# Optimization experiments

Measured on AMD Instinct MI355X. Metric: run time of the kernel, lower is better.

The kernel has to match this reference:

```python
import jax, jax.numpy as jnp
import numpy as np

N, E = 50000, 800000
F_IN, H, P, C = 128, 64, 16, 40
L = 3  # gcn_layers


def setup_inputs() -> dict:
    key = jax.random.key(0)
    ks = jax.random.split(key, 10)
    s = 0.05
    return {
        "x_h": jax.random.normal(ks[0], (N, F_IN), jnp.float32),
        "pos_feat": jax.random.normal(ks[1], (N, P), jnp.float32),
        "edge_index": jax.random.randint(ks[2], (2, E), 0, N, dtype=jnp.int32),
        "W_pos": jax.random.normal(ks[3], (P, H), jnp.float32) * s,
        "b_pos": jnp.zeros((H,), jnp.float32),
        "W_init": jax.random.normal(ks[4], (F_IN, H), jnp.float32) * s,
        "b_init": jnp.zeros((H,), jnp.float32),
        "W_l": jax.random.normal(ks[5], (L, H, H), jnp.float32) * s,  # neighbor weight
        "W_r": jax.random.normal(ks[6], (L, H, H), jnp.float32) * s,  # root weight
        "b_conv": jnp.zeros((L, H), jnp.float32),
        "W_last": jax.random.normal(ks[7], (H, C), jnp.float32) * s,
        "b_last": jnp.zeros((C,), jnp.float32),
    }


def _sage_conv(x, src, dst, Wl, Wr, b):
    # PyG SAGEConv(aggr='mean'): out_i = Wl @ mean_{j in N(i)} x_j + Wr @ x_i + b
    msgs = x[src]  # [E, H] gather of source-node features
    agg = jax.ops.segment_sum(msgs, dst, num_segments=N)
    cnt = jax.ops.segment_sum(jnp.ones((E,), x.dtype), dst, num_segments=N)
    agg = agg / jnp.clip(cnt, 1.0, None)[:, None]  # mean; deg-0 nodes -> 0
    return agg @ Wl + x @ Wr + b


def reference(x_h, pos_feat, edge_index, W_pos, b_pos, W_init, b_init,
              W_l, W_r, b_conv, W_last, b_last):
    src, dst = edge_index[0], edge_index[1]
    # pos_embedding -> (hyperbolic encode simplified to identity in Euclidean manifold) -> tanh
    hyp_pos = jnp.tanh(pos_feat @ W_pos + b_pos)  # [N, H]
    h = x_h @ W_init + b_init  # [N, H]
    for i in range(L):
        h = _sage_conv(h, src, dst, W_l[i], W_r[i], b_conv[i])
        if i != L - 1:
            h = h + hyp_pos       # run_base == 'False' branch
            h = jax.nn.relu(h)    # dropout is no-op in eval mode
    emb = h @ W_last + b_last     # [N, C]
    return emb, jax.nn.log_softmax(emb, axis=1)
```

## Files before the change

### kernel.cpp

```cpp
#include <hip/hip_runtime.h>
#include <hip/hip_bf16.h>

#define NN 50000
#define NE 800000
#define FIN 128
#define HD 64
#define NC 40
#define XG   782
#define NB   391
#define NBK  782
#define BW   64
#define BSTR 2048
#define GGRID 1563

typedef __hip_bfloat16 bf16;
typedef __attribute__((ext_vector_type(8))) short bf16x8;
typedef __attribute__((ext_vector_type(4))) float f32x4;

__device__ __forceinline__ void acc8(float* a, uint4 v){
  a[0] += __uint_as_float(v.x << 16); a[1] += __uint_as_float(v.x & 0xffff0000u);
  a[2] += __uint_as_float(v.y << 16); a[3] += __uint_as_float(v.y & 0xffff0000u);
  a[4] += __uint_as_float(v.z << 16); a[5] += __uint_as_float(v.z & 0xffff0000u);
  a[6] += __uint_as_float(v.w << 16); a[7] += __uint_as_float(v.w & 0xffff0000u);
}

__device__ __forceinline__ unsigned pack2(float lo, float hi){
  union { bf16 b; unsigned short u; } a, b;
  a.b = __float2bfloat16(lo);
  b.b = __float2bfloat16(hi);
  return (unsigned)a.u | ((unsigned)b.u << 16);
}

__device__ __forceinline__ short f2bf_bits(float f){
  union { bf16 b; short s; } u;
  u.b = __float2bfloat16(f);
  return u.s;
}

__device__ __forceinline__ void init_body(
    int wid, const float* __restrict__ x, const float* __restrict__ pos,
    const float* __restrict__ Wi, const float* __restrict__ bi,
    const float* __restrict__ Wp, const float* __restrict__ bp,
    bf16* __restrict__ h0b, bf16* __restrict__ hypb, int lane){
  const int quad = lane >> 4;
  const int col  = lane & 15;
  const int nw   = XG * 4;

  bf16x8 wif[4][4];
  #pragma unroll
  for (int ct = 0; ct < 4; ++ct)
    #pragma unroll
    for (int kf = 0; kf < 4; ++kf)
      #pragma unroll
      for (int j = 0; j < 8; ++j)
        wif[ct][kf][j] = f2bf_bits(Wi[(kf*32 + quad*8 + j)*HD + ct*16 + col]);
  bf16x8 wpf[4];
  #pragma unroll
  for (int ct = 0; ct < 4; ++ct)
    #pragma unroll
    for (int j = 0; j < 8; ++j){
      const int k = quad*8 + j;
      wpf[ct][j] = (k < 16) ? f2bf_bits(Wp[k*HD + ct*16 + col]) : (short)0;
    }
  float bih[4], bph[4];
  #pragma unroll
  for (int c = 0; c < 4; ++c){ bih[c] = bi[c*16 + col]; bph[c] = bp[c*16 + col]; }

  for (int t = wid; t < NN/16; t += nw){
    const int n0 = t * 16;
    bf16x8 af[4];
    #pragma unroll
    for (int kf = 0; kf < 4; ++kf){
      const float* xr = x + (size_t)(n0 + col)*FIN + kf*32 + quad*8;
      const float4 f0 = *(const float4*)xr;
      const float4 f1 = *(const float4*)(xr + 4);
      af[kf][0] = f2bf_bits(f0.x); af[kf][1] = f2bf_bits(f0.y);
      af[kf][2] = f2bf_bits(f0.z); af[kf][3] = f2bf_bits(f0.w);
      af[kf][4] = f2bf_bits(f1.x); af[kf][5] = f2bf_bits(f1.y);
      af[kf][6] = f2bf_bits(f1.z); af[kf][7] = f2bf_bits(f1.w);
    }
    bf16x8 ap;
    #pragma unroll
    for (int j = 0; j < 8; ++j) ap[j] = 0;
    if (quad < 2){
      const float* pr = pos + (size_t)(n0 + col)*16 + quad*8;
      const float4 p0 = *(const float4*)pr;
      const float4 p1 = *(const float4*)(pr + 4);
      ap[0] = f2bf_bits(p0.x); ap[1] = f2bf_bits(p0.y);
      ap[2] = f2bf_bits(p0.z); ap[3] = f2bf_bits(p0.w);
      ap[4] = f2bf_bits(p1.x); ap[5] = f2bf_bits(p1.y);
      ap[6] = f2bf_bits(p1.z); ap[7] = f2bf_bits(p1.w);
    }
    f32x4 ah[4], app[4];
    #pragma unroll
    for (int c = 0; c < 4; ++c){
      ah[c]  = (f32x4){bih[c], bih[c], bih[c], bih[c]};
      app[c] = (f32x4){bph[c], bph[c], bph[c], bph[c]};
    }
    #pragma unroll
    for (int ct = 0; ct < 4; ++ct){
      #pragma unroll
      for (int kf = 0; kf < 4; ++kf)
        ah[ct] = __builtin_amdgcn_mfma_f32_16x16x32_bf16(af[kf], wif[ct][kf], ah[ct], 0, 0, 0);
      app[ct] = __builtin_amdgcn_mfma_f32_16x16x32_bf16(ap, wpf[ct], app[ct], 0, 0, 0);
    }
    #pragma unroll
    for (int reg = 0; reg < 4; ++reg){
      const int n = n0 + quad*4 + reg;
      #pragma unroll
      for (int c = 0; c < 4; ++c){
        h0b[(size_t)n*HD + c*16 + col]  = __float2bfloat16(ah[c][reg]);
        hypb[(size_t)n*HD + c*16 + col] = __float2bfloat16(tanhf(app[c][reg]));
      }
    }
  }
}

__global__ __launch_bounds__(256) void k_hist(
    const int* __restrict__ ei, int* __restrict__ histT,
    const float* __restrict__ x, const float* __restrict__ pos,
    const float* __restrict__ Wi, const float* __restrict__ bi,
    const float* __restrict__ Wp, const float* __restrict__ bp,
    bf16* __restrict__ h0b, bf16* __restrict__ hypb){
  __shared__ int lh[NBK];
  if (blockIdx.x < NB){
    for (int i = threadIdx.x; i < NBK; i += 256) lh[i] = 0;
    __syncthreads();
    int e = blockIdx.x * 2048 + threadIdx.x;
    #pragma unroll
    for (int j = 0; j < 8; ++j, e += 256)
      if (e < NE) atomicAdd(&lh[ei[NE + e] >> 6], 1);
    __syncthreads();
    for (int i = threadIdx.x; i < NBK; i += 256)
      histT[blockIdx.x*NBK + i] = lh[i];
    return;
  }
  init_body((blockIdx.x - NB) * 4 + (threadIdx.x >> 6),
            x, pos, Wi, bi, Wp, bp, h0b, hypb, threadIdx.x & 63);
}

__global__ __launch_bounds__(512) void k_scanA(
    const int* __restrict__ histT, int* __restrict__ ofsT,
    int* __restrict__ totals){
  __shared__ int sc[512];
  const int b = blockIdx.x;
  const int t = threadIdx.x;
  const int v = (t < NB) ? histT[t*NBK + b] : 0;
  sc[t] = v; __syncthreads();
  for (int off = 1; off < 512; off <<= 1){
    const int xv = (t >= off) ? sc[t - off] : 0;
    __syncthreads();
    sc[t] += xv;
    __syncthreads();
  }
  if (t < NB) ofsT[t*NBK + b] = sc[t] - v;
  if (t == 511) totals[b] = sc[511];
}

__global__ __launch_bounds__(256) void k_scatter(
    const int* __restrict__ ei, const int* __restrict__ ofsT,
    int* __restrict__ packed){
  __shared__ int cur[NBK];
  for (int i = threadIdx.x; i < NBK; i += 256)
    cur[i] = (i << 11) + ofsT[blockIdx.x*NBK + i];
  __syncthreads();
  int e = blockIdx.x * 2048 + threadIdx.x;
  #pragma unroll
  for (int j = 0; j < 8; ++j, e += 256){
    if (e < NE){
      const int d = ei[NE + e];
      const int s = ei[e];
      const int b = d >> 6;
      const int p = atomicAdd(&cur[b], 1);
      if (p < ((b + 1) << 11))
        packed[p] = s | ((d & 63) << 16);
    }
  }
}

__global__ __launch_bounds__(256) void k_ell(
    const int* __restrict__ packed, const int* __restrict__ totals,
    unsigned short* __restrict__ esrc, int* __restrict__ degp){
  __shared__ int cnt[BW];
  __shared__ unsigned short ell[BW * 64];
  if (threadIdx.x < BW) cnt[threadIdx.x] = 0;
  __syncthreads();
  const int b  = blockIdx.x;
  const int lo = b << 11;
  const int hi = lo + totals[b];
  for (int e = lo + threadIdx.x; e < hi; e += 256){
    const int pk = packed[e];
    const int dl = (pk >> 16) & 63;
    const int p  = atomicAdd(&cnt[dl], 1);
    if (p < 64) ell[dl*64 + p] = (unsigned short)(pk & 0xffff);
  }
  __syncthreads();
  const int n0 = b * BW;
  for (int i = threadIdx.x; i < BW * 8; i += 256){
    const int node = i >> 3;
    if (n0 + node < NN)
      ((uint4*)(esrc + (size_t)(n0 + node)*64))[i & 7] = ((const uint4*)ell)[i];
  }
  for (int i = threadIdx.x; i < BW; i += 256)
    if (n0 + i < NN) degp[n0 + i] = min(cnt[i], 64);
}


__device__ __forceinline__ bf16x8 lds_frag(const unsigned int* hs, int r, int slot){
  union { uint4 u; bf16x8 v; } t;
  t.u = *(const uint4*)(hs + r*32 + ((slot ^ (r & 7)) << 2));
  return t.v;
}

__device__ __forceinline__ void gather_own_stage(
    const bf16* __restrict__ h, const int* __restrict__ degp,
    const unsigned short* __restrict__ esrc, unsigned int* hs){
  const int lane = threadIdx.x & 63;
  const int w    = threadIdx.x >> 6;
  const int grp  = lane >> 3;
  const int fq   = lane & 7;
  const int nl   = (w << 3) + grp;
  const int n    = (blockIdx.x << 5) + nl;
  const int ns   = (n < NN) ? n : 0;
  const int deg  = (n < NN) ? min(degp[n], 64) : 0;

  const uint4 hv = ((const uint4*)(h + (size_t)ns*HD))[fq];
  *(uint4*)(hs + 1024 + nl*32 + ((fq ^ (nl & 7)) << 2)) = hv;

  const uint4* er = (const uint4*)(esrc + ((size_t)ns << 6));
  float a[8] = {0,0,0,0,0,0,0,0};
  for (int eb = 0; eb < 64; eb += 8){
    if (!__any(eb < deg)) break;
    union { uint4 u; unsigned short s[8]; } ev;
    ev.u = er[eb >> 3];
    const int m = deg - eb;
    #pragma unroll
    for (int j = 0; j < 8; ++j){
      if (j < m){
        const uint4 v = ((const uint4*)(h + (size_t)ev.s[j]*HD))[fq];
        acc8(a, v);
      }
    }
  }
  const float inv = deg > 0 ? 1.f / (float)deg : 0.f;
  uint4 pv;
  pv.x = pack2(a[0]*inv, a[1]*inv);
  pv.y = pack2(a[2]*inv, a[3]*inv);
  pv.z = pack2(a[4]*inv, a[5]*inv);
  pv.w = pack2(a[6]*inv, a[7]*inv);
  *(uint4*)(hs + nl*32 + ((fq ^ (nl & 7)) << 2)) = pv;
}

__global__ __launch_bounds__(256) void k_g(
    const bf16* __restrict__ h, const int* __restrict__ degp,
    const unsigned short* __restrict__ esrc,
    const float* __restrict__ Wl, const float* __restrict__ Wr,
    const float* __restrict__ bc, const bf16* __restrict__ hypb,
    bf16* __restrict__ ho){
  __shared__ unsigned int hs[2048];
  const int lane = threadIdx.x & 63;
  const int w    = threadIdx.x >> 6;
  const int quad = lane >> 4;
  const int col  = lane & 15;
  const int tile = w & 1;
  const int ch   = w >> 1;

  bf16x8 fw[2][4];
  float zb[2];
  #pragma unroll
  for (int c = 0; c < 2; ++c){
    const int nc = (ch*2 + c)*16 + col;
    zb[c] = bc[nc];
    #pragma unroll
    for (int kf = 0; kf < 4; ++kf)
      #pragma unroll
      for (int j = 0; j < 8; ++j){
        const int k = kf*32 + quad*8 + j;
        fw[c][kf][j] = f2bf_bits((k < 64) ? Wl[k*HD + nc] : Wr[(k - 64)*HD + nc]);
      }
  }

  gather_own_stage(h, degp, esrc, hs);
  __syncthreads();

  const int r = tile*16 + col;
  const bf16x8 a0 = lds_frag(hs, r, quad);
  const bf16x8 a1 = lds_frag(hs, r, quad + 4);
  const bf16x8 a2 = lds_frag(hs + 1024, r, quad);
  const bf16x8 a3 = lds_frag(hs + 1024, r, quad + 4);
  __syncthreads();

  const int n0b = blockIdx.x << 5;
  unsigned short* st = (unsigned short*)hs;
  f32x4 acc[2];
  #pragma unroll
  for (int c = 0; c < 2; ++c){
    acc[c] = (f32x4){zb[c], zb[c], zb[c], zb[c]};
    acc[c] = __builtin_amdgcn_mfma_f32_16x16x32_bf16(a0, fw[c][0], acc[c], 0, 0, 0);
    acc[c] = __builtin_amdgcn_mfma_f32_16x16x32_bf16(a1, fw[c][1], acc[c], 0, 0, 0);
    acc[c] = __builtin_amdgcn_mfma_f32_16x16x32_bf16(a2, fw[c][2], acc[c], 0, 0, 0);
    acc[c] = __builtin_amdgcn_mfma_f32_16x16x32_bf16(a3, fw[c][3], acc[c], 0, 0, 0);
  }
  #pragma unroll
  for (int reg = 0; reg < 4; ++reg){
    const int rr = tile*16 + quad*4 + reg;
    const int nn = n0b + rr;
    #pragma unroll
    for (int c = 0; c < 2; ++c){
      const int oc = (ch*2 + c)*16 + col;
      float v = acc[c][reg];
      if (nn < NN) v += __bfloat162float(hypb[(size_t)nn*HD + oc]);
      v = fmaxf(v, 0.f);
      st[rr*64 + (((oc >> 3) ^ (rr & 7)) << 3) + (oc & 7)] = (unsigned short)f2bf_bits(v);
    }
  }
  __syncthreads();
  const int grp = lane >> 3;
  const int fq  = lane & 7;
  const int nl  = (w << 3) + grp;
  const int n   = n0b + nl;
  if (n < NN)
    ((uint4*)(ho + (size_t)n*HD))[fq] = *(const uint4*)(hs + nl*32 + ((fq ^ (nl & 7)) << 2));
}

__global__ __launch_bounds__(256) void k_gf(
    const bf16* __restrict__ h, const int* __restrict__ degp,
    const unsigned short* __restrict__ esrc,
    const float* __restrict__ Wl, const float* __restrict__ Wr,
    const float* __restrict__ bc,
    const float* __restrict__ Wlast, const float* __restrict__ blast,
    float* __restrict__ out){
  __shared__ unsigned int hs[2048];
  const int lane = threadIdx.x & 63;
  const int w    = threadIdx.x >> 6;
  const int quad = lane >> 4;
  const int col  = lane & 15;
  const int tile = w & 1;
  const int ch   = w >> 1;

  bf16x8 fw[2][4];
  float zb[2];
  #pragma unroll
  for (int c = 0; c < 2; ++c){
    const int nc = (ch*2 + c)*16 + col;
    zb[c] = bc[nc];
    #pragma unroll
    for (int kf = 0; kf < 4; ++kf)
      #pragma unroll
      for (int j = 0; j < 8; ++j){
        const int k = kf*32 + quad*8 + j;
        fw[c][kf][j] = f2bf_bits((k < 64) ? Wl[k*HD + nc] : Wr[(k - 64)*HD + nc]);
      }
  }

  gather_own_stage(h, degp, esrc, hs);
  __syncthreads();

  const int r = tile*16 + col;
  const bf16x8 a0 = lds_frag(hs, r, quad);
  const bf16x8 a1 = lds_frag(hs, r, quad + 4);
  const bf16x8 a2 = lds_frag(hs + 1024, r, quad);
  const bf16x8 a3 = lds_frag(hs + 1024, r, quad + 4);
  __syncthreads();

  const int n0b = blockIdx.x << 5;
  unsigned short* st = (unsigned short*)hs;
  f32x4 acc[2];
  #pragma unroll
  for (int c = 0; c < 2; ++c){
    acc[c] = (f32x4){zb[c], zb[c], zb[c], zb[c]};
    acc[c] = __builtin_amdgcn_mfma_f32_16x16x32_bf16(a0, fw[c][0], acc[c], 0, 0, 0);
    acc[c] = __builtin_amdgcn_mfma_f32_16x16x32_bf16(a1, fw[c][1], acc[c], 0, 0, 0);
    acc[c] = __builtin_amdgcn_mfma_f32_16x16x32_bf16(a2, fw[c][2], acc[c], 0, 0, 0);
    acc[c] = __builtin_amdgcn_mfma_f32_16x16x32_bf16(a3, fw[c][3], acc[c], 0, 0, 0);
  }
  #pragma unroll
  for (int reg = 0; reg < 4; ++reg){
    const int rr = tile*16 + quad*4 + reg;
    #pragma unroll
    for (int c = 0; c < 2; ++c){
      const int oc = (ch*2 + c)*16 + col;
      st[rr*64 + (((oc >> 3) ^ (rr & 7)) << 3) + (oc & 7)] =
          (unsigned short)f2bf_bits(acc[c][reg]);
    }
  }
  __syncthreads();
  if (w >= 2) return;

  bf16x8 wf[3][2];
  float bb[3];
  #pragma unroll
  for (int ct = 0; ct < 3; ++ct){
    const int nc = ct*16 + col;
    const bool valid = nc < NC;
    bb[ct] = valid ? blast[nc] : -1e30f;
    #pragma unroll
    for (int kf = 0; kf < 2; ++kf)
      #pragma unroll
      for (int j = 0; j < 8; ++j)
        wf[ct][kf][j] = valid ? f2bf_bits(Wlast[(kf*32 + quad*8 + j)*NC + nc]) : (short)0;
  }
  const int r2 = w*16 + col;
  const bf16x8 b0 = lds_frag(hs, r2, quad);
  const bf16x8 b1 = lds_frag(hs, r2, quad + 4);
  f32x4 ac[3];
  #pragma unroll
  for (int ct = 0; ct < 3; ++ct){
    ac[ct] = (f32x4){bb[ct], bb[ct], bb[ct], bb[ct]};
    ac[ct] = __builtin_amdgcn_mfma_f32_16x16x32_bf16(b0, wf[ct][0], ac[ct], 0, 0, 0);
    ac[ct] = __builtin_amdgcn_mfma_f32_16x16x32_bf16(b1, wf[ct][1], ac[ct], 0, 0, 0);
  }
  #pragma unroll
  for (int reg = 0; reg < 4; ++reg){
    const float e0 = ac[0][reg], e1 = ac[1][reg], e2 = ac[2][reg];
    float vmax = fmaxf(fmaxf(e0, e1), e2);
    vmax = fmaxf(vmax, __shfl_xor(vmax, 1, 64));
    vmax = fmaxf(vmax, __shfl_xor(vmax, 2, 64));
    vmax = fmaxf(vmax, __shfl_xor(vmax, 4, 64));
    vmax = fmaxf(vmax, __shfl_xor(vmax, 8, 64));
    float s = __expf(e0 - vmax) + __expf(e1 - vmax) + __expf(e2 - vmax);
    s += __shfl_xor(s, 1, 64);
    s += __shfl_xor(s, 2, 64);
    s += __shfl_xor(s, 4, 64);
    s += __shfl_xor(s, 8, 64);
    const float off = vmax + __logf(s);
    const int n = n0b + w*16 + quad*4 + reg;
    if (n < NN){
      #pragma unroll
      for (int ct = 0; ct < 3; ++ct){
        const int nc = ct*16 + col;
        if (nc < NC){
          const float e = ac[ct][reg];
          out[(size_t)n*NC + nc]                 = e;
          out[(size_t)NN*NC + (size_t)n*NC + nc] = e - off;
        }
      }
    }
  }
}

extern "C" void kernel_launch(void* const* d_in, const int* in_sizes, int n_in,
                              void* d_out, int out_size, void* d_ws, size_t ws_size,
                              hipStream_t stream){
  (void)in_sizes; (void)n_in; (void)out_size; (void)ws_size;
  const float* x_h    = (const float*)d_in[0];
  const float* pos    = (const float*)d_in[1];
  const int*   ei     = (const int*)  d_in[2];
  const float* W_pos  = (const float*)d_in[3];
  const float* b_pos  = (const float*)d_in[4];
  const float* W_init = (const float*)d_in[5];
  const float* b_init = (const float*)d_in[6];
  const float* W_l    = (const float*)d_in[7];
  const float* W_r    = (const float*)d_in[8];
  const float* b_conv = (const float*)d_in[9];
  const float* W_last = (const float*)d_in[10];
  const float* b_last = (const float*)d_in[11];
  float* out = (float*)d_out;

  char* p = (char*)d_ws;
  auto alloc = [&](size_t bytes)->char*{
    char* r = p; p += (bytes + 255) & ~(size_t)255; return r;
  };
  bf16* buf0 = (bf16*)alloc((size_t)NN*HD*2);
  bf16* buf1 = (bf16*)alloc((size_t)NN*HD*2);
  bf16* hypb = (bf16*)alloc((size_t)NN*HD*2);
  unsigned short* esrc = (unsigned short*)alloc((size_t)NN*64*2);
  int* degp   = (int*)alloc((size_t)NN*4);
  int* histT  = (int*)alloc((size_t)NB*NBK*4);
  int* ofsT   = (int*)alloc((size_t)NB*NBK*4);
  int* totals = (int*)alloc((size_t)NBK*4);
  int* packed = (int*)alloc((size_t)NBK*BSTR*4);

  k_hist   <<<NB + XG, 256, 0, stream>>>(ei, histT, x_h, pos,
                                         W_init, b_init, W_pos, b_pos, buf0, hypb);
  k_scanA  <<<NBK, 512, 0, stream>>>(histT, ofsT, totals);
  k_scatter<<<NB, 256, 0, stream>>>(ei, ofsT, packed);
  k_ell    <<<NBK, 256, 0, stream>>>(packed, totals, esrc, degp);

  k_g  <<<GGRID, 256, 0, stream>>>(buf0, degp, esrc,
                                   W_l + 0*HD*HD, W_r + 0*HD*HD, b_conv + 0*HD,
                                   hypb, buf1);
  k_g  <<<GGRID, 256, 0, stream>>>(buf1, degp, esrc,
                                   W_l + 1*HD*HD, W_r + 1*HD*HD, b_conv + 1*HD,
                                   hypb, buf0);
  k_gf <<<GGRID, 256, 0, stream>>>(buf0, degp, esrc,
                                   W_l + 2*HD*HD, W_r + 2*HD*HD, b_conv + 2*HD,
                                   W_last, b_last, out);
}
```

Before: 240.7 us.

## Fuse three SAGE layer kernels into one persistent kernel with grid barriers

Replaces the three per-layer kernel launches with a single persistent kernel of 512 blocks that loops over the node tiles and uses a software grid-wide barrier between layers. It removes two launches and the drain/fill gaps between them, and weights are loaded once per block rather than per tile. In exchange, parallelism drops from 1563 blocks to 512 with grid-stride loops, and correctness depends on all 512 blocks being co-resident, since the spin barrier deadlocks otherwise.

```diff
diff --git a/kernel.cpp b/kernel.cpp
--- a/kernel.cpp
+++ b/kernel.cpp
@@ -12,6 +12,7 @@
 #define BW   64
 #define BSTR 2048
 #define GGRID 1563
+#define LGRID 512
 
 typedef __hip_bfloat16 bf16;
 typedef __attribute__((ext_vector_type(8))) short bf16x8;
@@ -35,6 +36,24 @@
   union { bf16 b; short s; } u;
   u.b = __float2bfloat16(f);
   return u.s;
+}
+
+__device__ __forceinline__ void gridbar(int* bar, int* gen, const int nblk){
+  __syncthreads();
+  if (threadIdx.x == 0){
+    __threadfence();
+    const int g = __hip_atomic_load(gen, __ATOMIC_RELAXED, __HIP_MEMORY_SCOPE_AGENT);
+    const int v = __hip_atomic_fetch_add(bar, 1, __ATOMIC_ACQ_REL, __HIP_MEMORY_SCOPE_AGENT);
+    if (v == nblk - 1){
+      __hip_atomic_store(bar, 0, __ATOMIC_RELAXED, __HIP_MEMORY_SCOPE_AGENT);
+      __hip_atomic_fetch_add(gen, 1, __ATOMIC_RELEASE, __HIP_MEMORY_SCOPE_AGENT);
+    } else {
+      while (__hip_atomic_load(gen, __ATOMIC_RELAXED, __HIP_MEMORY_SCOPE_AGENT) == g)
+        __builtin_amdgcn_s_sleep(2);
+    }
+    __threadfence();
+  }
+  __syncthreads();
 }
 
 __device__ __forceinline__ void init_body(
@@ -205,7 +224,6 @@
     if (n0 + i < NN) degp[n0 + i] = min(cnt[i], 64);
 }
 
-
 __device__ __forceinline__ bf16x8 lds_frag(const unsigned int* hs, int r, int slot){
   union { uint4 u; bf16x8 v; } t;
   t.u = *(const uint4*)(hs + r*32 + ((slot ^ (r & 7)) << 2));
@@ -214,13 +232,13 @@
 
 __device__ __forceinline__ void gather_own_stage(
     const bf16* __restrict__ h, const int* __restrict__ degp,
-    const unsigned short* __restrict__ esrc, unsigned int* hs){
+    const unsigned short* __restrict__ esrc, unsigned int* hs, int tb){
   const int lane = threadIdx.x & 63;
   const int w    = threadIdx.x >> 6;
   const int grp  = lane >> 3;
   const int fq   = lane & 7;
   const int nl   = (w << 3) + grp;
-  const int n    = (blockIdx.x << 5) + nl;
+  const int n    = (tb << 5) + nl;
   const int ns   = (n < NN) ? n : 0;
   const int deg  = (n < NN) ? min(degp[n], 64) : 0;
 
@@ -251,13 +269,12 @@
   *(uint4*)(hs + nl*32 + ((fq ^ (nl & 7)) << 2)) = pv;
 }
 
-__global__ __launch_bounds__(256) void k_g(
-    const bf16* __restrict__ h, const int* __restrict__ degp,
+__device__ __forceinline__ void layer_body(
+    unsigned int* hs, const bf16* __restrict__ h, const int* __restrict__ degp,
     const unsigned short* __restrict__ esrc,
     const float* __restrict__ Wl, const float* __restrict__ Wr,
     const float* __restrict__ bc, const bf16* __restrict__ hypb,
     bf16* __restrict__ ho){
-  __shared__ unsigned int hs[2048];
   const int lane = threadIdx.x & 63;
   const int w    = threadIdx.x >> 6;
   const int quad = lane >> 4;
@@ -280,161 +297,173 @@
       }
   }
 
-  gather_own_stage(h, degp, esrc, hs);
-  __syncthreads();
-
-  const int r = tile*16 + col;
-  const bf16x8 a0 = lds_frag(hs, r, quad);
-  const bf16x8 a1 = lds_frag(hs, r, quad + 4);
-  const bf16x8 a2 = lds_frag(hs + 1024, r, quad);
-  const bf16x8 a3 = lds_frag(hs + 1024, r, quad + 4);
-  __syncthreads();
-
-  const int n0b = blockIdx.x << 5;
-  unsigned short* st = (unsigned short*)hs;
-  f32x4 acc[2];
-  #pragma unroll
-  for (int c = 0; c < 2; ++c){
-    acc[c] = (f32x4){zb[c], zb[c], zb[c], zb[c]};
-    acc[c] = __builtin_amdgcn_mfma_f32_16x16x32_bf16(a0, fw[c][0], acc[c], 0, 0, 0);
-    acc[c] = __builtin_amdgcn_mfma_f32_16x16x32_bf16(a1, fw[c][1], acc[c], 0, 0, 0);
-    acc[c] = __builtin_amdgcn_mfma_f32_16x16x32_bf16(a2, fw[c][2], acc[c], 0, 0, 0);
-    acc[c] = __builtin_amdgcn_mfma_f32_16x16x32_bf16(a3, fw[c][3], acc[c], 0, 0, 0);
-  }
-  #pragma unroll
-  for (int reg = 0; reg < 4; ++reg){
-    const int rr = tile*16 + quad*4 + reg;
-    const int nn = n0b + rr;
+  for (int tb = blockIdx.x; tb < GGRID; tb += LGRID){
+    gather_own_stage(h, degp, esrc, hs, tb);
+    __syncthreads();
+    const int r = tile*16 + col;
+    const bf16x8 a0 = lds_frag(hs, r, quad);
+    const bf16x8 a1 = lds_frag(hs, r, quad + 4);
+    const bf16x8 a2 = lds_frag(hs + 1024, r, quad);
+    const bf16x8 a3 = lds_frag(hs + 1024, r, quad + 4);
+    __syncthreads();
+
+    const int n0b = tb << 5;
+    unsigned short* st = (unsigned short*)hs;
+    f32x4 acc[2];
     #pragma unroll
     for (int c = 0; c < 2; ++c){
-      const int oc = (ch*2 + c)*16 + col;
-      float v = acc[c][reg];
-      if (nn < NN) v += __bfloat162float(hypb[(size_t)nn*HD + oc]);
-      v = fmaxf(v, 0.f);
-      st[rr*64 + (((oc >> 3) ^ (rr & 7)) << 3) + (oc & 7)] = (unsigned short)f2bf_bits(v);
-    }
-  }
-  __syncthreads();
-  const int grp = lane >> 3;
-  const int fq  = lane & 7;
-  const int nl  = (w << 3) + grp;
-  const int n   = n0b + nl;
-  if (n < NN)
-    ((uint4*)(ho + (size_t)n*HD))[fq] = *(const uint4*)(hs + nl*32 + ((fq ^ (nl & 7)) << 2));
-}
-
-__global__ __launch_bounds__(256) void k_gf(
-    const bf16* __restrict__ h, const int* __restrict__ degp,
+      acc[c] = (f32x4){zb[c], zb[c], zb[c], zb[c]};
+      acc[c] = __builtin_amdgcn_mfma_f32_16x16x32_bf16(a0, fw[c][0], acc[c], 0, 0, 0);
+      acc[c] = __builtin_amdgcn_mfma_f32_16x16x32_bf16(a1, fw[c][1], acc[c], 0, 0, 0);
+      acc[c] = __builtin_amdgcn_mfma_f32_16x16x32_bf16(a2, fw[c][2], acc[c], 0, 0, 0);
+      acc[c] = __builtin_amdgcn_mfma_f32_16x16x32_bf16(a3, fw[c][3], acc[c], 0, 0, 0);
+    }
+    #pragma unroll
+    for (int reg = 0; reg < 4; ++reg){
+      const int rr = tile*16 + quad*4 + reg;
+      const int nn = n0b + rr;
+      #pragma unroll
+      for (int c = 0; c < 2; ++c){
+        const int oc = (ch*2 + c)*16 + col;
+        float v = acc[c][reg];
+        if (nn < NN) v += __bfloat162float(hypb[(size_t)nn*HD + oc]);
+        v = fmaxf(v, 0.f);
+        st[rr*64 + (((oc >> 3) ^ (rr & 7)) << 3) + (oc & 7)] = (unsigned short)f2bf_bits(v);
+      }
+    }
+    __syncthreads();
+    const int grp = lane >> 3;
+    const int fq  = lane & 7;
+    const int nl  = (w << 3) + grp;
+    const int n   = n0b + nl;
+    if (n < NN)
+      ((uint4*)(ho + (size_t)n*HD))[fq] = *(const uint4*)(hs + nl*32 + ((fq ^ (nl & 7)) << 2));
+    __syncthreads();
+  }
+}
+
+__global__ __launch_bounds__(256, 2) void k_layers(
+    bf16* h0, bf16* h1, const int* __restrict__ degp,
     const unsigned short* __restrict__ esrc,
     const float* __restrict__ Wl, const float* __restrict__ Wr,
-    const float* __restrict__ bc,
+    const float* __restrict__ bc, const bf16* __restrict__ hypb,
     const float* __restrict__ Wlast, const float* __restrict__ blast,
-    float* __restrict__ out){
+    float* __restrict__ out, int* bar, int* gen){
   __shared__ unsigned int hs[2048];
   const int lane = threadIdx.x & 63;
   const int w    = threadIdx.x >> 6;
   const int quad = lane >> 4;
   const int col  = lane & 15;
-  const int tile = w & 1;
-  const int ch   = w >> 1;
-
-  bf16x8 fw[2][4];
-  float zb[2];
-  #pragma unroll
-  for (int c = 0; c < 2; ++c){
-    const int nc = (ch*2 + c)*16 + col;
-    zb[c] = bc[nc];
-    #pragma unroll
-    for (int kf = 0; kf < 4; ++kf)
-      #pragma unroll
-      for (int j = 0; j < 8; ++j){
-        const int k = kf*32 + quad*8 + j;
-        fw[c][kf][j] = f2bf_bits((k < 64) ? Wl[k*HD + nc] : Wr[(k - 64)*HD + nc]);
-      }
-  }
-
-  gather_own_stage(h, degp, esrc, hs);
-  __syncthreads();
-
-  const int r = tile*16 + col;
-  const bf16x8 a0 = lds_frag(hs, r, quad);
-  const bf16x8 a1 = lds_frag(hs, r, quad + 4);
-  const bf16x8 a2 = lds_frag(hs + 1024, r, quad);
-  const bf16x8 a3 = lds_frag(hs + 1024, r, quad + 4);
-  __syncthreads();
-
-  const int n0b = blockIdx.x << 5;
-  unsigned short* st = (unsigned short*)hs;
-  f32x4 acc[2];
-  #pragma unroll
-  for (int c = 0; c < 2; ++c){
-    acc[c] = (f32x4){zb[c], zb[c], zb[c], zb[c]};
-    acc[c] = __builtin_amdgcn_mfma_f32_16x16x32_bf16(a0, fw[c][0], acc[c], 0, 0, 0);
-    acc[c] = __builtin_amdgcn_mfma_f32_16x16x32_bf16(a1, fw[c][1], acc[c], 0, 0, 0);
-    acc[c] = __builtin_amdgcn_mfma_f32_16x16x32_bf16(a2, fw[c][2], acc[c], 0, 0, 0);
-    acc[c] = __builtin_amdgcn_mfma_f32_16x16x32_bf16(a3, fw[c][3], acc[c], 0, 0, 0);
-  }
-  #pragma unroll
-  for (int reg = 0; reg < 4; ++reg){
-    const int rr = tile*16 + quad*4 + reg;
+
+  layer_body(hs, h0, degp, esrc, Wl + 0*HD*HD, Wr + 0*HD*HD, bc + 0*HD, hypb, h1);
+  gridbar(bar, gen, LGRID);
+  layer_body(hs, h1, degp, esrc, Wl + 1*HD*HD, Wr + 1*HD*HD, bc + 1*HD, hypb, h0);
+  gridbar(bar, gen, LGRID);
+
+  {
+    const int tile = w & 1;
+    const int ch   = w >> 1;
+    bf16x8 fw[2][4];
+    float zb[2];
     #pragma unroll
     for (int c = 0; c < 2; ++c){
-      const int oc = (ch*2 + c)*16 + col;
-      st[rr*64 + (((oc >> 3) ^ (rr & 7)) << 3) + (oc & 7)] =
-          (unsigned short)f2bf_bits(acc[c][reg]);
-    }
-  }
-  __syncthreads();
-  if (w >= 2) return;
-
-  bf16x8 wf[3][2];
-  float bb[3];
-  #pragma unroll
-  for (int ct = 0; ct < 3; ++ct){
-    const int nc = ct*16 + col;
-    const bool valid = nc < NC;
-    bb[ct] = valid ? blast[nc] : -1e30f;
-    #pragma unroll
-    for (int kf = 0; kf < 2; ++kf)
-      #pragma unroll
-      for (int j = 0; j < 8; ++j)
-        wf[ct][kf][j] = valid ? f2bf_bits(Wlast[(kf*32 + quad*8 + j)*NC + nc]) : (short)0;
-  }
-  const int r2 = w*16 + col;
-  const bf16x8 b0 = lds_frag(hs, r2, quad);
-  const bf16x8 b1 = lds_frag(hs, r2, quad + 4);
-  f32x4 ac[3];
-  #pragma unroll
-  for (int ct = 0; ct < 3; ++ct){
-    ac[ct] = (f32x4){bb[ct], bb[ct], bb[ct], bb[ct]};
-    ac[ct] = __builtin_amdgcn_mfma_f32_16x16x32_bf16(b0, wf[ct][0], ac[ct], 0, 0, 0);
-    ac[ct] = __builtin_amdgcn_mfma_f32_16x16x32_bf16(b1, wf[ct][1], ac[ct], 0, 0, 0);
-  }
-  #pragma unroll
-  for (int reg = 0; reg < 4; ++reg){
-    const float e0 = ac[0][reg], e1 = ac[1][reg], e2 = ac[2][reg];
-    float vmax = fmaxf(fmaxf(e0, e1), e2);
-    vmax = fmaxf(vmax, __shfl_xor(vmax, 1, 64));
-    vmax = fmaxf(vmax, __shfl_xor(vmax, 2, 64));
-    vmax = fmaxf(vmax, __shfl_xor(vmax, 4, 64));
-    vmax = fmaxf(vmax, __shfl_xor(vmax, 8, 64));
-    float s = __expf(e0 - vmax) + __expf(e1 - vmax) + __expf(e2 - vmax);
-    s += __shfl_xor(s, 1, 64);
-    s += __shfl_xor(s, 2, 64);
-    s += __shfl_xor(s, 4, 64);
-    s += __shfl_xor(s, 8, 64);
-    const float off = vmax + __logf(s);
-    const int n = n0b + w*16 + quad*4 + reg;
-    if (n < NN){
-      #pragma unroll
-      for (int ct = 0; ct < 3; ++ct){
-        const int nc = ct*16 + col;
-        if (nc < NC){
-          const float e = ac[ct][reg];
-          out[(size_t)n*NC + nc]                 = e;
-          out[(size_t)NN*NC + (size_t)n*NC + nc] = e - off;
+      const int nc = (ch*2 + c)*16 + col;
+      zb[c] = bc[2*HD + nc];
+      #pragma unroll
+      for (int kf = 0; kf < 4; ++kf)
+        #pragma unroll
+        for (int j = 0; j < 8; ++j){
+          const int k = kf*32 + quad*8 + j;
+          fw[c][kf][j] = f2bf_bits((k < 64) ? Wl[2*HD*HD + k*HD + nc]
+                                            : Wr[2*HD*HD + (k - 64)*HD + nc]);
         }
-      }
+    }
+    bf16x8 wf[3][2];
+    float bb[3];
+    #pragma unroll
+    for (int ct = 0; ct < 3; ++ct){
+      const int nc = ct*16 + col;
+      const bool valid = nc < NC;
+      bb[ct] = valid ? blast[nc] : -1e30f;
+      #pragma unroll
+      for (int kf = 0; kf < 2; ++kf)
+        #pragma unroll
+        for (int j = 0; j < 8; ++j)
+          wf[ct][kf][j] = valid ? f2bf_bits(Wlast[(kf*32 + quad*8 + j)*NC + nc]) : (short)0;
+    }
+
+    for (int tb = blockIdx.x; tb < GGRID; tb += LGRID){
+      gather_own_stage(h0, degp, esrc, hs, tb);
+      __syncthreads();
+      const int r = tile*16 + col;
+      const bf16x8 a0 = lds_frag(hs, r, quad);
+      const bf16x8 a1 = lds_frag(hs, r, quad + 4);
+      const bf16x8 a2 = lds_frag(hs + 1024, r, quad);
+      const bf16x8 a3 = lds_frag(hs + 1024, r, quad + 4);
+      __syncthreads();
+
+      const int n0b = tb << 5;
+      unsigned short* st = (unsigned short*)hs;
+      f32x4 acc[2];
+      #pragma unroll
+      for (int c = 0; c < 2; ++c){
+        acc[c] = (f32x4){zb[c], zb[c], zb[c], zb[c]};
+        acc[c] = __builtin_amdgcn_mfma_f32_16x16x32_bf16(a0, fw[c][0], acc[c], 0, 0, 0);
+        acc[c] = __builtin_amdgcn_mfma_f32_16x16x32_bf16(a1, fw[c][1], acc[c], 0, 0, 0);
+        acc[c] = __builtin_amdgcn_mfma_f32_16x16x32_bf16(a2, fw[c][2], acc[c], 0, 0, 0);
+        acc[c] = __builtin_amdgcn_mfma_f32_16x16x32_bf16(a3, fw[c][3], acc[c], 0, 0, 0);
+      }
+      #pragma unroll
+      for (int reg = 0; reg < 4; ++reg){
+        const int rr = tile*16 + quad*4 + reg;
+        #pragma unroll
+        for (int c = 0; c < 2; ++c){
+          const int oc = (ch*2 + c)*16 + col;
+          st[rr*64 + (((oc >> 3) ^ (rr & 7)) << 3) + (oc & 7)] =
+              (unsigned short)f2bf_bits(acc[c][reg]);
+        }
+      }
+      __syncthreads();
+      if (w < 2){
+        const int r2 = w*16 + col;
+        const bf16x8 b0 = lds_frag(hs, r2, quad);
+        const bf16x8 b1 = lds_frag(hs, r2, quad + 4);
+        f32x4 ac[3];
+        #pragma unroll
+        for (int ct = 0; ct < 3; ++ct){
+          ac[ct] = (f32x4){bb[ct], bb[ct], bb[ct], bb[ct]};
+          ac[ct] = __builtin_amdgcn_mfma_f32_16x16x32_bf16(b0, wf[ct][0], ac[ct], 0, 0, 0);
+          ac[ct] = __builtin_amdgcn_mfma_f32_16x16x32_bf16(b1, wf[ct][1], ac[ct], 0, 0, 0);
+        }
+        #pragma unroll
+        for (int reg = 0; reg < 4; ++reg){
+          const float e0 = ac[0][reg], e1 = ac[1][reg], e2 = ac[2][reg];
+          float vmax = fmaxf(fmaxf(e0, e1), e2);
+          vmax = fmaxf(vmax, __shfl_xor(vmax, 1, 64));
+          vmax = fmaxf(vmax, __shfl_xor(vmax, 2, 64));
+          vmax = fmaxf(vmax, __shfl_xor(vmax, 4, 64));
+          vmax = fmaxf(vmax, __shfl_xor(vmax, 8, 64));
+          float s = __expf(e0 - vmax) + __expf(e1 - vmax) + __expf(e2 - vmax);
+          s += __shfl_xor(s, 1, 64);
+          s += __shfl_xor(s, 2, 64);
+          s += __shfl_xor(s, 4, 64);
+          s += __shfl_xor(s, 8, 64);
+          const float off = vmax + __logf(s);
+          const int n = n0b + w*16 + quad*4 + reg;
+          if (n < NN){
+            #pragma unroll
+            for (int ct = 0; ct < 3; ++ct){
+              const int nc = ct*16 + col;
+              if (nc < NC){
+                const float e = ac[ct][reg];
+                out[(size_t)n*NC + nc]                 = e;
+                out[(size_t)NN*NC + (size_t)n*NC + nc] = e - off;
+              }
+            }
+          }
+        }
+      }
+      __syncthreads();
     }
   }
 }
@@ -470,6 +499,9 @@
   int* ofsT   = (int*)alloc((size_t)NB*NBK*4);
   int* totals = (int*)alloc((size_t)NBK*4);
   int* packed = (int*)alloc((size_t)NBK*BSTR*4);
+  int* barrier= (int*)alloc(256);
+
+  hipMemsetAsync(barrier, 0, 8, stream);
 
   k_hist   <<<NB + XG, 256, 0, stream>>>(ei, histT, x_h, pos,
                                          W_init, b_init, W_pos, b_pos, buf0, hypb);
@@ -477,13 +509,7 @@
   k_scatter<<<NB, 256, 0, stream>>>(ei, ofsT, packed);
   k_ell    <<<NBK, 256, 0, stream>>>(packed, totals, esrc, degp);
 
-  k_g  <<<GGRID, 256, 0, stream>>>(buf0, degp, esrc,
-                                   W_l + 0*HD*HD, W_r + 0*HD*HD, b_conv + 0*HD,
-                                   hypb, buf1);
-  k_g  <<<GGRID, 256, 0, stream>>>(buf1, degp, esrc,
-                                   W_l + 1*HD*HD, W_r + 1*HD*HD, b_conv + 1*HD,
-                                   hypb, buf0);
-  k_gf <<<GGRID, 256, 0, stream>>>(buf0, degp, esrc,
-                                   W_l + 2*HD*HD, W_r + 2*HD*HD, b_conv + 2*HD,
-                                   W_last, b_last, out);
-}
+  k_layers <<<LGRID, 256, 0, stream>>>(buf0, buf1, degp, esrc,
+                                       W_l, W_r, b_conv, hypb,
+                                       W_last, b_last, out, barrier, barrier + 1);
+}
```

After: 439.7 us. 82.7% more time.
